# Kernel optimization log

Measured on AMD Instinct MI355X. Metric: run time of the kernel, lower is better.

Reference implementation:

```python
import jax, jax.numpy as jnp
import numpy as np
from jax.scipy.special import logsumexp

B, DK, N, M = 16, 512, 1024, 1024
SINKHORN_ITERS = 5
EPS = 1e-8


def setup_inputs() -> dict:
    key = jax.random.key(0)
    k1, k2, k3, k4, k5 = jax.random.split(key, 5)
    return {
        "src_embedding": jax.random.normal(k1, (B, DK, N), dtype=jnp.float32),
        "tgt_embedding": jax.random.normal(k2, (B, DK, M), dtype=jnp.float32),
        "src": jax.random.normal(k3, (B, 3, N), dtype=jnp.float32),
        "tgt": jax.random.normal(k4, (B, 3, M), dtype=jnp.float32),
        # temperature must be positive; uniform in [0.05, 1.0)
        "temperature": jax.random.uniform(k5, (B,), dtype=jnp.float32, minval=0.05, maxval=1.0),
    }


def sinkhorn(scores, n_iters):
    # ZeroPad2d((0,1,0,1)): pad one slack row and one slack column with zeros
    scores = jnp.pad(scores, ((0, 0), (0, 1), (0, 1)))
    for _ in range(n_iters):
        # row normalization (all rows except slack row)
        top = scores[:, :-1, :] - logsumexp(scores[:, :-1, :], axis=2, keepdims=True)
        scores = jnp.concatenate([top, scores[:, -1:, :]], axis=1)
        # column normalization (all cols except slack col)
        left = scores[:, :, :-1] - logsumexp(scores[:, :, :-1], axis=1, keepdims=True)
        scores = jnp.concatenate([left, scores[:, :, -1:]], axis=2)
    return scores[:, :-1, :-1]


def reference(src_embedding, tgt_embedding, src, tgt, temperature):
    b, d_k, n = src_embedding.shape
    # [B, N, M] similarity scores
    dists = jnp.einsum('bdn,bdm->bnm', src_embedding, tgt_embedding) / jnp.sqrt(jnp.float32(d_k))
    affinity = dists / temperature[:, None, None]
    log_perm = sinkhorn(affinity, SINKHORN_ITERS)
    perm = jnp.exp(log_perm)                                             # [B,N,M]
    perm_norm = perm / (jnp.sum(perm, axis=2, keepdims=True) + EPS)      # [B,N,M]
    # soft correspondence: weighted_tgt[b,:,i] = sum_j perm_norm[b,i,j] * tgt[b,:,j]
    weighted_tgt = jnp.einsum('bdm,bnm->bdn', tgt, perm_norm)            # [B,3,N]
    weights = jnp.sum(perm, axis=-1, keepdims=True)                      # [B,N,1]
    weights_norm = weights / (jnp.sum(weights, axis=1, keepdims=True) + EPS)
    weights_norm = jnp.swapaxes(weights_norm, 1, 2)                      # [B,1,N]
    src_centroid = jnp.sum(src * weights_norm, axis=2, keepdims=True)    # [B,3,1]
    tgt_centroid = jnp.sum(weighted_tgt * weights_norm, axis=2, keepdims=True)
    src_centered = src - src_centroid
    corr_centered = (weighted_tgt - tgt_centroid) * weights_norm
    # weighted cross-covariance, batched 3x3
    H = jnp.einsum('bin,bjn->bij', src_centered, corr_centered)          # [B,3,3]
    # batched Procrustes via SVD (torch.svd: H = u diag(s) v^T; jnp: H = u diag(s) vh)
    u, s, vh = jnp.linalg.svd(H)
    v = jnp.swapaxes(vh, 1, 2)
    ut = jnp.swapaxes(u, 1, 2)
    r = jnp.matmul(v, ut)
    r_det = jnp.linalg.det(r)                                            # [B]
    diag = jnp.stack([jnp.ones_like(r_det), jnp.ones_like(r_det), r_det], axis=-1)  # [B,3]
    R = jnp.matmul(v * diag[:, None, :], ut)                             # [B,3,3]
    t = (jnp.matmul(-R, src_centroid) + tgt_centroid).reshape(b, 3)
    return R, t, perm_norm
```

## Files before the change

### kernel.cpp

```cpp
#include <hip/hip_runtime.h>
#include <math.h>

#define BB 16
#define NN 1024
#define MM 1024
#define DKK 512
#define RBLK 16
#define NRB  (NN/RBLK)
#define LSTR 1032

typedef short short8 __attribute__((ext_vector_type(8)));
typedef float f32x4 __attribute__((ext_vector_type(4)));

__device__ float g_u[BB*NN];
__device__ float g_v[BB*MM];
__device__ float g_w[BB*NN];
__device__ float g_wt[BB*3*NN];
__device__ float g_pm[BB*NRB*MM];
__device__ float g_ps[BB*NRB*MM];
__device__ __attribute__((aligned(16))) unsigned short gAh[BB*NN*DKK];
__device__ __attribute__((aligned(16))) unsigned short gAl[BB*NN*DKK];
__device__ __attribute__((aligned(16))) unsigned short gBh[BB*MM*DKK];
__device__ __attribute__((aligned(16))) unsigned short gBl[BB*MM*DKK];

__device__ __forceinline__ unsigned int bf16_rne(float x){
    unsigned int u = __float_as_uint(x);
    return (u + 0x7fffu + ((u>>16)&1u)) >> 16;
}

__device__ __forceinline__ void gl_lds(const void* g, void* l){
    __builtin_amdgcn_global_load_lds(
        (const __attribute__((address_space(1))) unsigned int*)g,
        (__attribute__((address_space(3))) unsigned int*)l, 16, 0, 0);
}

__global__ __launch_bounds__(256) void convert_split(const float* __restrict__ A,
                                                     const float* __restrict__ Bm) {
    int z = blockIdx.z;
    int which = z >> 4;
    int b = z & 15;
    int t = threadIdx.x;
    if (z == 0 && blockIdx.y == 0){
        *(float4*)(g_v + blockIdx.x*1024 + t*4) = make_float4(0.f,0.f,0.f,0.f);
    }
    const float* X = which ? Bm : A;
    unsigned short* Hh = which ? gBh : gAh;
    unsigned short* Hl = which ? gBl : gAl;
    int d0 = blockIdx.y * 64;
    int i0 = blockIdx.x * 64;
    __shared__ float T[64*65];
    const float* Xb = X + ((size_t)b*DKK + d0)*NN + i0;
#pragma unroll
    for (int it=0; it<4; ++it){
        int lin = t + 256*it;
        int d = lin >> 4;
        int i4 = lin & 15;
        float4 v = *(const float4*)(Xb + (size_t)d*NN + i4*4);
        T[(i4*4+0)*65 + d] = v.x;
        T[(i4*4+1)*65 + d] = v.y;
        T[(i4*4+2)*65 + d] = v.z;
        T[(i4*4+3)*65 + d] = v.w;
    }
    __syncthreads();
    size_t obase = ((size_t)b*NN + i0)*DKK + d0;
#pragma unroll
    for (int it=0; it<2; ++it){
        int c = t + 256*it;
        int i = c >> 3;
        int p = c & 7;
        unsigned int hw[4], lw[4];
#pragma unroll
        for (int j=0;j<4;j++){
            float x0 = T[i*65 + p*8 + 2*j];
            float x1 = T[i*65 + p*8 + 2*j+1];
            unsigned int h0 = bf16_rne(x0);
            unsigned int h1 = bf16_rne(x1);
            float hf0 = __uint_as_float(h0<<16);
            float hf1 = __uint_as_float(h1<<16);
            unsigned int l0 = bf16_rne(x0 - hf0);
            unsigned int l1 = bf16_rne(x1 - hf1);
            hw[j] = h0 | (h1<<16);
            lw[j] = l0 | (l1<<16);
        }
        int pw = (p & 4) | ((p + (i>>1)) & 3);
        size_t eo = obase + (size_t)i*DKK + pw*8;
        uint4 hv; hv.x=hw[0]; hv.y=hw[1]; hv.z=hw[2]; hv.w=hw[3];
        uint4 lv; lv.x=lw[0]; lv.y=lw[1]; lv.z=lw[2]; lv.w=lw[3];
        *(uint4*)(Hh + eo) = hv;
        *(uint4*)(Hl + eo) = lv;
    }
}

__global__ __launch_bounds__(512,2) void gemm_mfma(const float* __restrict__ temp,
                                                   float* __restrict__ C) {
    int id   = blockIdx.x;
    int xcd  = id & 7;
    int slot = id >> 3;
    int b    = xcd*2 + (slot >> 4);
    int sub  = slot & 15;
    int i0   = (sub >> 2) << 8;
    int j0   = (sub & 3) << 8;
    __shared__ __attribute__((aligned(16))) char lds[131072];
    int t = threadIdx.x;
    int lane = t & 63, w = t >> 6;
    int wr = w >> 2, wc = w & 3;

    int rql = lane >> 2, cl = lane & 3;
    unsigned eoff = (unsigned)(b * (NN*DKK*2));
    unsigned offA = eoff + (unsigned)((i0 + w*32 + rql)*1024) + (unsigned)(cl*16);
    unsigned offB = eoff + (unsigned)((j0 + w*32 + rql)*1024) + (unsigned)(cl*16);
    int dq0 = w*2048;

    const char* pAh = (const char*)gAh;
    const char* pAl = (const char*)gAl;
    const char* pBh = (const char*)gBh;
    const char* pBl = (const char*)gBl;

    f32x4 acc[32];
#pragma unroll
    for (int q=0;q<32;q++) acc[q] = (f32x4){0.f,0.f,0.f,0.f};

    int fslot = ((lane>>4) + ((lane&15)>>1)) & 3;
    int faoff = (wr*128 + (lane&15))*64 + fslot*16;
    int fboff = (wc*64  + (lane&15))*64 + fslot*16;

    gl_lds(pAh + offA,          lds + 0      + dq0);
    gl_lds(pAh + offA + 16384,  lds + 0      + dq0 + 1024);
    gl_lds(pBh + offB,          lds + 65536  + dq0);
    gl_lds(pBh + offB + 16384,  lds + 65536  + dq0 + 1024);
    gl_lds(pAl + offA,          lds + 32768  + dq0);
    gl_lds(pAl + offA + 16384,  lds + 32768  + dq0 + 1024);
    gl_lds(pBl + offB,          lds + 98304  + dq0);
    gl_lds(pBl + offB + 16384,  lds + 98304  + dq0 + 1024);

    short8 ah[8], bh[4], al[8], bl[4];

    for (int ks=0; ks<16; ++ks){
        int par = (ks & 1) << 14;
        int nxt = 16384 - par;

        asm volatile("s_waitcnt vmcnt(4)" ::: "memory");
        __builtin_amdgcn_s_barrier();
        __builtin_amdgcn_sched_barrier(0);
        {
            const char* fa = lds + par + faoff;
            const char* fb = lds + 65536 + par + fboff;
#pragma unroll
            for (int mf=0;mf<8;mf++) ah[mf] = *(const short8*)(fa + mf*1024);
#pragma unroll
            for (int nf=0;nf<4;nf++) bh[nf] = *(const short8*)(fb + nf*1024);
        }
        if (ks < 15){
            offA += 64; offB += 64;
            gl_lds(pAh + offA,         lds + 0     + nxt + dq0);
            gl_lds(pAh + offA + 16384, lds + 0     + nxt + dq0 + 1024);
            gl_lds(pBh + offB,         lds + 65536 + nxt + dq0);
            gl_lds(pBh + offB + 16384, lds + 65536 + nxt + dq0 + 1024);
        }
        asm volatile("s_waitcnt lgkmcnt(0)" ::: "memory");
        __builtin_amdgcn_sched_barrier(0);
        __builtin_amdgcn_s_setprio(1);
#pragma unroll
        for (int nf=0;nf<4;nf++)
#pragma unroll
            for (int mf=0;mf<8;mf++)
                acc[mf*4+nf] = __builtin_amdgcn_mfma_f32_16x16x32_bf16(ah[mf], bh[nf], acc[mf*4+nf], 0,0,0);
        __builtin_amdgcn_s_setprio(0);
        __builtin_amdgcn_sched_barrier(0);

        if (ks < 15) asm volatile("s_waitcnt vmcnt(6)" ::: "memory");
        else         asm volatile("s_waitcnt vmcnt(2)" ::: "memory");
        __builtin_amdgcn_s_barrier();
        __builtin_amdgcn_sched_barrier(0);
        {
            const char* fa = lds + 32768 + par + faoff;
#pragma unroll
            for (int mf=0;mf<8;mf++) al[mf] = *(const short8*)(fa + mf*1024);
        }
        if (ks < 15){
            gl_lds(pAl + offA,         lds + 32768 + nxt + dq0);
            gl_lds(pAl + offA + 16384, lds + 32768 + nxt + dq0 + 1024);
        }
        asm volatile("s_waitcnt lgkmcnt(0)" ::: "memory");
        __builtin_amdgcn_sched_barrier(0);
        __builtin_amdgcn_s_setprio(1);
#pragma unroll
        for (int nf=0;nf<4;nf++)
#pragma unroll
            for (int mf=0;mf<8;mf++)
                acc[mf*4+nf] = __builtin_amdgcn_mfma_f32_16x16x32_bf16(al[mf], bh[nf], acc[mf*4+nf], 0,0,0);
        __builtin_amdgcn_s_setprio(0);
        __builtin_amdgcn_sched_barrier(0);

        if (ks < 15) asm volatile("s_waitcnt vmcnt(6)" ::: "memory");
        else         asm volatile("s_waitcnt vmcnt(0)" ::: "memory");
        __builtin_amdgcn_s_barrier();
        __builtin_amdgcn_sched_barrier(0);
        {
            const char* fb = lds + 98304 + par + fboff;
#pragma unroll
            for (int nf=0;nf<4;nf++) bl[nf] = *(const short8*)(fb + nf*1024);
        }
        if (ks < 15){
            gl_lds(pBl + offB,         lds + 98304 + nxt + dq0);
            gl_lds(pBl + offB + 16384, lds + 98304 + nxt + dq0 + 1024);
        }
        asm volatile("s_waitcnt lgkmcnt(0)" ::: "memory");
        __builtin_amdgcn_sched_barrier(0);
        __builtin_amdgcn_s_setprio(1);
#pragma unroll
        for (int nf=0;nf<4;nf++)
#pragma unroll
            for (int mf=0;mf<8;mf++)
                acc[mf*4+nf] = __builtin_amdgcn_mfma_f32_16x16x32_bf16(ah[mf], bl[nf], acc[mf*4+nf], 0,0,0);
        __builtin_amdgcn_s_setprio(0);
        __builtin_amdgcn_sched_barrier(0);
    }

    float scale = 1.0f/(22.62741699796952f * temp[b]);
    float* Cb = C + ((size_t)b<<20);
    int r0c = i0 + wr*128 + ((lane>>4)<<2);
    int c0c = j0 + wc*64 + (lane&15);
#pragma unroll
    for (int mf=0;mf<8;mf++){
#pragma unroll
        for (int r2=0;r2<4;r2++){
            float* rowp = Cb + (size_t)(r0c + mf*16 + r2)*MM + c0c;
#pragma unroll
            for (int nf=0;nf<4;nf++)
                rowp[nf*16] = acc[mf*4+nf][r2]*scale;
        }
    }
}

__global__ __launch_bounds__(256) void sink_iter(const float* __restrict__ S) {
    int b   = blockIdx.y;
    int rb  = blockIdx.x;
    int row0 = rb*RBLK;
    int t = threadIdx.x;
    __shared__ float Ls[RBLK*LSTR];
    __shared__ float v_l[1024];
    __shared__ float u_l[RBLK];

    float4 v4 = *(const float4*)(g_v + (b<<10) + t*4);
    *(float4*)(v_l + t*4) = v4;

    const float* Sb = S + ((size_t)b*NN + row0)*MM;
#pragma unroll
    for (int rr=0; rr<RBLK; ++rr){
        float4 s4 = *(const float4*)(Sb + (size_t)rr*MM + t*4);
        s4.x -= v4.x; s4.y -= v4.y; s4.z -= v4.z; s4.w -= v4.w;
        *(float4*)(&Ls[rr*LSTR + t*4]) = s4;
    }
    __syncthreads();

    {
        int r = t >> 4, c = t & 15;
        const float* Lr = &Ls[r*LSTR + c];
        float m = -INFINITY;
#pragma unroll
        for (int k=0;k<64;k++) m = fmaxf(m, Lr[16*k]);
#pragma unroll
        for (int off=1; off<16; off<<=1) m = fmaxf(m, __shfl_xor(m, off));
        m = fmaxf(m, 0.0f);
        float s = 0.0f;
#pragma unroll
        for (int k=0;k<64;k++) s += __expf(Lr[16*k] - m);
#pragma unroll
        for (int off=1; off<16; off<<=1) s += __shfl_xor(s, off);
        s += __expf(-m);
        float u = m + __logf(s);
        if (c==0){ u_l[r] = u; g_u[b*NN + row0 + r] = u; }
    }
    __syncthreads();

    float mm[4], ss[4];
#pragma unroll
    for (int q=0;q<4;q++){ mm[q]=-INFINITY; ss[q]=0.f; }
#pragma unroll
    for (int r=0;r<RBLK;++r){
        float ur = u_l[r];
        const float* Lr = &Ls[r*LSTR];
#pragma unroll
        for (int q=0;q<4;q++)
            mm[q] = fmaxf(mm[q], Lr[t + 256*q] - ur);
    }
#pragma unroll
    for (int r=0;r<RBLK;++r){
        float ur = u_l[r];
        const float* Lr = &Ls[r*LSTR];
#pragma unroll
        for (int q=0;q<4;q++)
            ss[q] += __expf(Lr[t + 256*q] - ur - mm[q]);
    }
    size_t pbase = ((size_t)(b*NRB + rb) << 10) + t;
#pragma unroll
    for (int q=0;q<4;q++){
        g_pm[pbase + 256*q] = mm[q] + v_l[t + 256*q];
        g_ps[pbase + 256*q] = ss[q];
    }
}

__global__ __launch_bounds__(64) void col_lse_combine() {
    int idx = blockIdx.x*64 + threadIdx.x;
    int b = idx >> 10; int j = idx & (MM-1);
    size_t base = ((size_t)(b*NRB) << 10) + j;
    float m[8], s[8];
#pragma unroll
    for (int k=0;k<8;k++){ m[k] = -INFINITY; s[k] = 0.0f; }
    for (int c=0;c<NRB;c+=8){
#pragma unroll
        for (int k=0;k<8;k++){
            float om = g_pm[base + ((size_t)(c+k)<<10)];
            float os = g_ps[base + ((size_t)(c+k)<<10)];
            float nm = fmaxf(m[k], om);
            s[k] = s[k]*__expf(m[k]-nm) + os*__expf(om-nm);
            m[k] = nm;
        }
    }
#pragma unroll
    for (int st=1; st<8; st<<=1){
#pragma unroll
        for (int k=0;k<8;k+=2*st){
            float nm = fmaxf(m[k], m[k+st]);
            s[k] = s[k]*__expf(m[k]-nm) + s[k+st]*__expf(m[k+st]-nm);
            m[k] = nm;
        }
    }
    float nm = fmaxf(m[0], 0.0f);
    float Sx = s[0]*__expf(m[0]-nm) + __expf(-nm);
    g_v[idx] = nm + __logf(Sx);
}

__global__ __launch_bounds__(256) void finalize_rows(float* __restrict__ S,
                                                     const float* __restrict__ tgt) {
    int row  = blockIdx.x*4 + (threadIdx.x>>6);
    int lane = threadIdx.x & 63;
    int b = row >> 10;
    int i = row & (NN-1);
    float ui = g_u[row];
    float4* srow = (float4*)(S + (size_t)row*MM);
    const float4* vb = (const float4*)(g_v + (b<<10));
    const float4* t0 = (const float4*)(tgt + (size_t)b*3*MM);
    const float4* t1 = (const float4*)(tgt + (size_t)b*3*MM + MM);
    const float4* t2 = (const float4*)(tgt + (size_t)b*3*MM + 2*MM);
    float p[16];
    float rs=0.f, a0=0.f, a1=0.f, a2=0.f;
#pragma unroll
    for (int k=0;k<4;k++){
        float4 s4 = srow[lane + 64*k];
        float4 v4 = vb[lane + 64*k];
        p[4*k+0] = __expf(s4.x - ui - v4.x);
        p[4*k+1] = __expf(s4.y - ui - v4.y);
        p[4*k+2] = __expf(s4.z - ui - v4.z);
        p[4*k+3] = __expf(s4.w - ui - v4.w);
        rs += p[4*k+0]+p[4*k+1]+p[4*k+2]+p[4*k+3];
        float4 w0 = t0[lane + 64*k];
        float4 w1 = t1[lane + 64*k];
        float4 w2 = t2[lane + 64*k];
        a0 += p[4*k+0]*w0.x + p[4*k+1]*w0.y + p[4*k+2]*w0.z + p[4*k+3]*w0.w;
        a1 += p[4*k+0]*w1.x + p[4*k+1]*w1.y + p[4*k+2]*w1.z + p[4*k+3]*w1.w;
        a2 += p[4*k+0]*w2.x + p[4*k+1]*w2.y + p[4*k+2]*w2.z + p[4*k+3]*w2.w;
    }
    for (int off=32; off; off>>=1){
        rs += __shfl_xor(rs, off);
        a0 += __shfl_xor(a0, off);
        a1 += __shfl_xor(a1, off);
        a2 += __shfl_xor(a2, off);
    }
    float inv = 1.0f/(rs + 1e-8f);
#pragma unroll
    for (int k=0;k<4;k++){
        srow[lane + 64*k] = make_float4(p[4*k+0]*inv, p[4*k+1]*inv, p[4*k+2]*inv, p[4*k+3]*inv);
    }
    if (lane==0){
        g_w[row] = rs;
        g_wt[(b*3+0)*NN + i] = a0*inv;
        g_wt[(b*3+1)*NN + i] = a1*inv;
        g_wt[(b*3+2)*NN + i] = a2*inv;
    }
}

__global__ __launch_bounds__(256) void procrustes(const float* __restrict__ src,
                                                  float* __restrict__ out) {
    int b = blockIdx.x;
    int t = threadIdx.x;
    int lane = t & 63, w = t >> 6;
    __shared__ float part[4][16];
    const float* wrow = g_w + b*NN;
    const float* sb  = src  + (size_t)b*3*NN;
    const float* wtb = g_wt + (size_t)b*3*NN;

    float wv[4], sv[3][4], tv3[3][4];
#pragma unroll
    for (int k=0;k<4;k++){
        int i = t + 256*k;
        wv[k] = wrow[i];
#pragma unroll
        for (int c=0;c<3;c++){
            sv[c][k]  = sb[c*NN+i];
            tv3[c][k] = wtb[c*NN+i];
        }
    }

    auto block_reduce = [&](float* v, int nv){
        for (int jx=0;jx<nv;jx++){
            float x = v[jx];
            for (int off=32;off;off>>=1) x += __shfl_xor(x, off);
            if (lane==0) part[w][jx] = x;
        }
        __syncthreads();
        for (int jx=0;jx<nv;jx++)
            v[jx] = part[0][jx]+part[1][jx]+part[2][jx]+part[3][jx];
        __syncthreads();
    };

    float W = wv[0]+wv[1]+wv[2]+wv[3];
    block_reduce(&W, 1);
    float winv = 1.0f/(W + 1e-8f);
    float wn[4];
#pragma unroll
    for (int k=0;k<4;k++) wn[k] = wv[k]*winv;

    float a[6];
#pragma unroll
    for (int c=0;c<3;c++){
        float p1=0.f,p2=0.f;
#pragma unroll
        for (int k=0;k<4;k++){ p1 += sv[c][k]*wn[k]; p2 += tv3[c][k]*wn[k]; }
        a[c]=p1; a[3+c]=p2;
    }
    block_reduce(a, 6);
    float sc[3], tc[3];
#pragma unroll
    for (int c=0;c<3;c++){ sc[c]=a[c]; tc[c]=a[3+c]; }

    float H[9];
#pragma unroll
    for (int c=0;c<3;c++)
#pragma unroll
        for (int d=0;d<3;d++){
            float p=0.f;
#pragma unroll
            for (int k=0;k<4;k++)
                p += (sv[c][k]-sc[c]) * ((tv3[d][k]-tc[d])*wn[k]);
            H[c*3+d]=p;
        }
    block_reduce(H, 9);

    if (t==0){
        double Hd[3][3];
        for (int r2=0;r2<3;r2++) for (int c2=0;c2<3;c2++) Hd[r2][c2]=H[r2*3+c2];
        double K[3][3];
        for (int i2=0;i2<3;i2++)
            for (int j2=0;j2<3;j2++){
                double acc=0;
                for (int r2=0;r2<3;r2++) acc += Hd[r2][i2]*Hd[r2][j2];
                K[i2][j2]=acc;
            }
        double V[3][3]={{1,0,0},{0,1,0},{0,0,1}};
        const int PQ[3][2]={{0,1},{0,2},{1,2}};
        for (int sweep=0; sweep<30; ++sweep){
            double off = fabs(K[0][1])+fabs(K[0][2])+fabs(K[1][2]);
            if (off < 1e-26) break;
            for (int pi=0; pi<3; ++pi){
                int p = PQ[pi][0], q = PQ[pi][1];
                double apq = K[p][q];
                if (fabs(apq) < 1e-300) continue;
                double tau = (K[q][q]-K[p][p])/(2.0*apq);
                double tt  = (tau>=0.0?1.0:-1.0)/(fabs(tau)+sqrt(1.0+tau*tau));
                double c   = 1.0/sqrt(1.0+tt*tt);
                double s   = tt*c;
                double Kpp=K[p][p], Kqq=K[q][q];
                K[p][p] = Kpp - tt*apq;
                K[q][q] = Kqq + tt*apq;
                K[p][q] = 0.0; K[q][p] = 0.0;
                int r2 = 3-p-q;
                double Krp=K[r2][p], Krq=K[r2][q];
                K[r2][p] = c*Krp - s*Krq; K[p][r2]=K[r2][p];
                K[r2][q] = s*Krp + c*Krq; K[q][r2]=K[r2][q];
                for (int rr=0; rr<3; ++rr){
                    double vp=V[rr][p], vq=V[rr][q];
                    V[rr][p] = c*vp - s*vq;
                    V[rr][q] = s*vp + c*vq;
                }
            }
        }
        double lam[3]={K[0][0],K[1][1],K[2][2]};
        int o0=0,o1=1,o2=2,tmp;
        if (lam[o0]<lam[o1]){tmp=o0;o0=o1;o1=tmp;}
        if (lam[o0]<lam[o2]){tmp=o0;o0=o2;o2=tmp;}
        if (lam[o1]<lam[o2]){tmp=o1;o1=o2;o2=tmp;}
        int ord[3]={o0,o1,o2};
        double Vs[3][3], U[3][3];
        for (int k=0;k<3;k++)
            for (int r2=0;r2<3;r2++) Vs[r2][k]=V[r2][ord[k]];
        for (int k=0;k<3;k++){
            double ux = Hd[0][0]*Vs[0][k] + Hd[0][1]*Vs[1][k] + Hd[0][2]*Vs[2][k];
            double uy = Hd[1][0]*Vs[0][k] + Hd[1][1]*Vs[1][k] + Hd[1][2]*Vs[2][k];
            double uz = Hd[2][0]*Vs[0][k] + Hd[2][1]*Vs[1][k] + Hd[2][2]*Vs[2][k];
            double n = sqrt(ux*ux+uy*uy+uz*uz);
            if (n > 1e-30){ U[0][k]=ux/n; U[1][k]=uy/n; U[2][k]=uz/n; }
            else {
                double cx = U[1][0]*U[2][1]-U[2][0]*U[1][1];
                double cy = U[2][0]*U[0][1]-U[0][0]*U[2][1];
                double cz = U[0][0]*U[1][1]-U[1][0]*U[0][1];
                U[0][k]=cx; U[1][k]=cy; U[2][k]=cz;
            }
        }
        double rm[3][3];
        for (int i2=0;i2<3;i2++)
            for (int j2=0;j2<3;j2++)
                rm[i2][j2] = Vs[i2][0]*U[j2][0] + Vs[i2][1]*U[j2][1] + Vs[i2][2]*U[j2][2];
        double det = rm[0][0]*(rm[1][1]*rm[2][2]-rm[1][2]*rm[2][1])
                   - rm[0][1]*(rm[1][0]*rm[2][2]-rm[1][2]*rm[2][0])
                   + rm[0][2]*(rm[1][0]*rm[2][1]-rm[1][1]*rm[2][0]);
        double R[3][3];
        for (int i2=0;i2<3;i2++)
            for (int j2=0;j2<3;j2++)
                R[i2][j2] = Vs[i2][0]*U[j2][0] + Vs[i2][1]*U[j2][1] + det*Vs[i2][2]*U[j2][2];
        double tvv[3];
        for (int i2=0;i2<3;i2++)
            tvv[i2] = -(R[i2][0]*sc[0]+R[i2][1]*sc[1]+R[i2][2]*sc[2]) + tc[i2];
        for (int i2=0;i2<3;i2++)
            for (int j2=0;j2<3;j2++)
                out[b*9 + i2*3 + j2] = (float)R[i2][j2];
        for (int i2=0;i2<3;i2++)
            out[144 + b*3 + i2] = (float)tvv[i2];
    }
}

extern "C" void kernel_launch(void* const* d_in, const int* in_sizes, int n_in,
                              void* d_out, int out_size, void* d_ws, size_t ws_size,
                              hipStream_t stream) {
    const float* src_emb = (const float*)d_in[0];
    const float* tgt_emb = (const float*)d_in[1];
    const float* src     = (const float*)d_in[2];
    const float* tgt     = (const float*)d_in[3];
    const float* temp    = (const float*)d_in[4];
    float* out = (float*)d_out;
    float* S = out + 192;

    hipLaunchKernelGGL(convert_split, dim3(16,8,32), dim3(256), 0, stream, src_emb, tgt_emb);
    hipLaunchKernelGGL(gemm_mfma, dim3(256), dim3(512), 0, stream, temp, S);
    for (int it=0; it<5; ++it){
        hipLaunchKernelGGL(sink_iter, dim3(NRB,BB), dim3(256), 0, stream, S);
        hipLaunchKernelGGL(col_lse_combine, dim3(256), dim3(64), 0, stream);
    }
    hipLaunchKernelGGL(finalize_rows, dim3(4096), dim3(256), 0, stream, S, tgt);
    hipLaunchKernelGGL(procrustes, dim3(16), dim3(256), 0, stream, src, out);
}
```

Baseline: 331.9 us.

## Fuse column LSE combine into sinkhorn row kernel, recomputing v per block

Each sinkhorn row-iteration block now reduces the per-row-block column max/sum partials itself to obtain the column potential v, instead of relying on a separate combine kernel. The first iteration uses v=0 directly, and only the final combine launch remains for the finalize stage. This removes four kernel launches and their global round-trips. In exchange, every block redundantly re-reads all 64 partial sets for its batch and runs a serial 64-step merge with exponentials.

```diff
diff --git a/kernel.cpp b/kernel.cpp
--- a/kernel.cpp
+++ b/kernel.cpp
@@ -40,9 +40,6 @@
     int which = z >> 4;
     int b = z & 15;
     int t = threadIdx.x;
-    if (z == 0 && blockIdx.y == 0){
-        *(float4*)(g_v + blockIdx.x*1024 + t*4) = make_float4(0.f,0.f,0.f,0.f);
-    }
     const float* X = which ? Bm : A;
     unsigned short* Hh = which ? gBh : gAh;
     unsigned short* Hl = which ? gBl : gAl;
@@ -233,7 +230,8 @@
     }
 }
 
-__global__ __launch_bounds__(256) void sink_iter(const float* __restrict__ S) {
+__global__ __launch_bounds__(256) void sink_iter(const float* __restrict__ S,
+                                                 int first) {
     int b   = blockIdx.y;
     int rb  = blockIdx.x;
     int row0 = rb*RBLK;
@@ -242,8 +240,34 @@
     __shared__ float v_l[1024];
     __shared__ float u_l[RBLK];
 
-    float4 v4 = *(const float4*)(g_v + (b<<10) + t*4);
-    *(float4*)(v_l + t*4) = v4;
+    if (first){
+        *(float4*)(v_l + t*4) = make_float4(0.f,0.f,0.f,0.f);
+    } else {
+        float m[4], s[4];
+#pragma unroll
+        for (int k=0;k<4;k++){ m[k] = -INFINITY; s[k] = 0.0f; }
+        size_t base = ((size_t)(b*NRB) << 10) + t;
+        for (int c=0;c<NRB;++c){
+            size_t o = base + ((size_t)c<<10);
+#pragma unroll
+            for (int k=0;k<4;k++){
+                float om = g_pm[o + 256*k];
+                float os = g_ps[o + 256*k];
+                float d  = om - m[k];
+                float e  = __expf(-fabsf(d));
+                if (d > 0.0f){ s[k] = s[k]*e + os; m[k] = om; }
+                else         { s[k] += os*e; }
+            }
+        }
+#pragma unroll
+        for (int k=0;k<4;k++){
+            float nm = fmaxf(m[k], 0.0f);
+            float Sx = s[k]*__expf(m[k]-nm) + __expf(-nm);
+            v_l[t + 256*k] = nm + __logf(Sx);
+        }
+    }
+    __syncthreads();
+    float4 v4 = *(const float4*)(v_l + t*4);
 
     const float* Sb = S + ((size_t)b*NN + row0)*MM;
 #pragma unroll
@@ -543,10 +567,10 @@
 
     hipLaunchKernelGGL(convert_split, dim3(16,8,32), dim3(256), 0, stream, src_emb, tgt_emb);
     hipLaunchKernelGGL(gemm_mfma, dim3(256), dim3(512), 0, stream, temp, S);
-    for (int it=0; it<5; ++it){
-        hipLaunchKernelGGL(sink_iter, dim3(NRB,BB), dim3(256), 0, stream, S);
-        hipLaunchKernelGGL(col_lse_combine, dim3(256), dim3(64), 0, stream);
-    }
+    hipLaunchKernelGGL(sink_iter, dim3(NRB,BB), dim3(256), 0, stream, S, 1);
+    for (int it=1; it<5; ++it)
+        hipLaunchKernelGGL(sink_iter, dim3(NRB,BB), dim3(256), 0, stream, S, 0);
+    hipLaunchKernelGGL(col_lse_combine, dim3(256), dim3(64), 0, stream);
     hipLaunchKernelGGL(finalize_rows, dim3(4096), dim3(256), 0, stream, S, tgt);
     hipLaunchKernelGGL(procrustes, dim3(16), dim3(256), 0, stream, src, out);
 }
```

Measured after the change: 434.0 us. 30.8% more time.
